# Kernel tuning notes

Hardware: AMD Instinct MI355X
Metric: run time of the kernel (lower is better)

## Reference

```python
import jax, jax.numpy as jnp
import numpy as np

R, C, B, E, H = 128, 256, 1, 768, 12
DK = E // H

def setup_inputs() -> dict:
    key = jax.random.key(0)
    ks = jax.random.split(key, 5)
    s = 1.0 / np.sqrt(E)
    return {
        "x": jax.random.normal(ks[0], (R, C, B, E), jnp.float32),
        "Wq": jax.random.normal(ks[1], (E, E), jnp.float32) * s,
        "bq": jnp.zeros((E,), jnp.float32),
        "Wk": jax.random.normal(ks[2], (E, E), jnp.float32) * s,
        "bk": jnp.zeros((E,), jnp.float32),
        "Wv": jax.random.normal(ks[3], (E, E), jnp.float32) * s,
        "bv": jnp.zeros((E,), jnp.float32),
        "Wo": jax.random.normal(ks[4], (E, E), jnp.float32) * s,
        "bo": jnp.zeros((E,), jnp.float32),
    }

def reference(x, Wq, bq, Wk, bk, Wv, bv, Wo, bo):
    n_rows, n_cols, batch, emb = x.shape
    scaling = (DK ** -0.5) / jnp.sqrt(jnp.float32(n_rows))
    # projections (torch Linear: x @ W.T + b)
    q = (x @ Wq.T + bq).reshape(n_rows, n_cols, batch, H, DK) * scaling
    k = (x @ Wk.T + bk).reshape(n_rows, n_cols, batch, H, DK)
    v = (x @ Wv.T + bv).reshape(n_rows, n_cols, batch, H, DK)
    # pooled attention logits: sum over rows r -> [H, B, C, C]
    attn = jnp.einsum('rinhd,rjnhd->hnij', q, k)
    probs = jax.nn.softmax(attn, axis=-1)  # single softmax shared across rows
    # context: [R, C, B, H, DK]
    c = jnp.einsum('hnij,rjnhd->rinhd', probs, v).reshape(n_rows, n_cols, batch, emb)
    out = c @ Wo.T + bo
    return out, probs
```

## Files before the change

### kernel.cpp

```cpp
#include <hip/hip_runtime.h>
#include <math.h>

#define R_  128
#define C_  256
#define E_  768
#define H_  12
#define DK_ 64
#define T_  (R_*C_)
#define RS_ 8
#define LP  40

typedef __attribute__((ext_vector_type(8))) short          bf16x8;
typedef __attribute__((ext_vector_type(4))) float          f32x4;
typedef __attribute__((ext_vector_type(4))) unsigned short u16x4;
typedef __attribute__((ext_vector_type(8))) unsigned short u16x8;

struct HL { unsigned short h, l; };

__device__ __forceinline__ HL split2(float f) {
    HL o;
    unsigned int u = __float_as_uint(f);
    o.h = (unsigned short)(u >> 16);
    float r = f - __uint_as_float(u & 0xFFFF0000u);
    o.l = (unsigned short)(__float_as_uint(r) >> 16);
    return o;
}

__device__ __forceinline__ void gload16(const void* g, void* l) {
    __builtin_amdgcn_global_load_lds(
        (const __attribute__((address_space(1))) unsigned int*)g,
        (__attribute__((address_space(3))) unsigned int*)l,
        16, 0, 0);
}

__global__ __launch_bounds__(256) void split_kernel(
    const float* __restrict__ src,
    unsigned short* __restrict__ h, unsigned short* __restrict__ l)
{
    const size_t i = ((size_t)blockIdx.x * 256 + threadIdx.x) * 8;
    float4 f0 = *(const float4*)(src + i);
    float4 f1 = *(const float4*)(src + i + 4);
    float v[8] = { f0.x, f0.y, f0.z, f0.w, f1.x, f1.y, f1.z, f1.w };
    u16x8 hh, ll;
    #pragma unroll
    for (int j = 0; j < 8; ++j) { HL e = split2(v[j]); hh[j] = e.h; ll[j] = e.l; }
    *(u16x8*)(h + i) = hh;
    *(u16x8*)(l + i) = ll;
}

template<int OMODE>
__global__ __launch_bounds__(256, 2) void gemm_kernel(
    const unsigned short* __restrict__ Ah, const unsigned short* __restrict__ Al,
    const unsigned short* __restrict__ Bh, const unsigned short* __restrict__ Bl,
    const float* __restrict__ bias, float scale,
    float* __restrict__ Y32, unsigned short* __restrict__ Yh, unsigned short* __restrict__ Yl)
{
    __shared__ __align__(16) unsigned short smem[16384];
    const unsigned short* AsH = smem;
    const unsigned short* AsL = smem + 4096;
    const unsigned short* BsH = smem + 8192;
    const unsigned short* BsL = smem + 12288;

    const int tid  = threadIdx.x;
    const int m0   = blockIdx.x * 128;
    const int n0   = blockIdx.y * 128;
    const int wave = tid >> 6, lane = tid & 63;
    const int wm   = (wave & 1) * 64, wn = (wave >> 1) * 64;
    const int fr   = lane & 15;
    const int kqs  = (((lane >> 4) ^ ((fr >> 1) & 3)) * 8);

    const int lrow = lane >> 2;
    const int gd   = (lane & 3) ^ ((lane >> 3) & 3);
    const unsigned short* gsrc = (wave == 0) ? Ah : (wave == 1) ? Al
                               : (wave == 2) ? Bh : Bl;
    const int rbase = (wave < 2) ? m0 : n0;
    unsigned short* lt = smem + wave * 4096;
    const unsigned short* sp = gsrc + (size_t)(rbase + lrow) * E_ + 8 * gd;

    f32x4 acc[4][4] = {};

    for (int k0 = 0; k0 < E_; k0 += 32) {
        #pragma unroll
        for (int i = 0; i < 8; ++i)
            gload16(sp + k0 + (size_t)i * 16 * E_, lt + i * 512);
        __syncthreads();

        bf16x8 a_h[4], a_l[4], b_h[4], b_l[4];
        #pragma unroll
        for (int t = 0; t < 4; ++t) {
            a_h[t] = *(const bf16x8*)&AsH[(wm + t * 16 + fr) * 32 + kqs];
            a_l[t] = *(const bf16x8*)&AsL[(wm + t * 16 + fr) * 32 + kqs];
            b_h[t] = *(const bf16x8*)&BsH[(wn + t * 16 + fr) * 32 + kqs];
            b_l[t] = *(const bf16x8*)&BsL[(wn + t * 16 + fr) * 32 + kqs];
        }
        #pragma unroll
        for (int i = 0; i < 4; ++i)
            #pragma unroll
            for (int j = 0; j < 4; ++j) {
                acc[i][j] = __builtin_amdgcn_mfma_f32_16x16x32_bf16(a_h[i], b_h[j], acc[i][j], 0, 0, 0);
                acc[i][j] = __builtin_amdgcn_mfma_f32_16x16x32_bf16(a_h[i], b_l[j], acc[i][j], 0, 0, 0);
                acc[i][j] = __builtin_amdgcn_mfma_f32_16x16x32_bf16(a_l[i], b_h[j], acc[i][j], 0, 0, 0);
            }
        __syncthreads();
    }

    float* rep = (float*)smem + wave * 1024;
    const int mr = lane >> 2;
    const int nc = (lane & 3) * 16;
    #pragma unroll
    for (int ti = 0; ti < 4; ++ti) {
        __syncthreads();
        #pragma unroll
        for (int tj = 0; tj < 4; ++tj)
            #pragma unroll
            for (int r = 0; r < 4; ++r)
                rep[((lane >> 4) * 4 + r) * 64 + tj * 16 + fr] = acc[ti][tj][r];
        __syncthreads();
        float v[16];
        #pragma unroll
        for (int c = 0; c < 4; ++c)
            *(float4*)&v[4 * c] = *(const float4*)&rep[mr * 64 + nc + 4 * c];
        const int gm = m0 + wm + ti * 16 + mr;
        const int gn = n0 + wn + nc;
        if constexpr (OMODE == 1) {
            #pragma unroll
            for (int c = 0; c < 4; ++c) {
                float4 bv = *(const float4*)&bias[gn + 4 * c];
                float4 o;
                o.x = (v[4*c+0] + bv.x) * scale; o.y = (v[4*c+1] + bv.y) * scale;
                o.z = (v[4*c+2] + bv.z) * scale; o.w = (v[4*c+3] + bv.w) * scale;
                *(float4*)&Y32[(size_t)gm * E_ + gn + 4 * c] = o;
            }
        } else {
            unsigned short hh[16], ll[16];
            #pragma unroll
            for (int c = 0; c < 4; ++c) {
                float4 bv = *(const float4*)&bias[gn + 4 * c];
                HL e0 = split2((v[4*c+0] + bv.x) * scale);
                HL e1 = split2((v[4*c+1] + bv.y) * scale);
                HL e2 = split2((v[4*c+2] + bv.z) * scale);
                HL e3 = split2((v[4*c+3] + bv.w) * scale);
                hh[4*c+0] = e0.h; ll[4*c+0] = e0.l;
                hh[4*c+1] = e1.h; ll[4*c+1] = e1.l;
                hh[4*c+2] = e2.h; ll[4*c+2] = e2.l;
                hh[4*c+3] = e3.h; ll[4*c+3] = e3.l;
            }
            u16x8 H0, H1, L0, L1;
            #pragma unroll
            for (int j = 0; j < 8; ++j) { H0[j] = hh[j]; H1[j] = hh[8+j]; L0[j] = ll[j]; L1[j] = ll[8+j]; }
            *(u16x8*)&Yh[(size_t)gm * E_ + gn]     = H0;
            *(u16x8*)&Yh[(size_t)gm * E_ + gn + 8] = H1;
            *(u16x8*)&Yl[(size_t)gm * E_ + gn]     = L0;
            *(u16x8*)&Yl[(size_t)gm * E_ + gn + 8] = L1;
        }
    }
}

__global__ __launch_bounds__(256, 2) void attn_mfma(
    const unsigned short* __restrict__ Qh, const unsigned short* __restrict__ Ql,
    const unsigned short* __restrict__ Kh, const unsigned short* __restrict__ Kl,
    float* __restrict__ part)
{
    __shared__ __align__(16) unsigned short smem[16384];
    const unsigned short* AsH = smem;
    const unsigned short* AsL = smem + 4096;
    const unsigned short* BsH = smem + 8192;
    const unsigned short* BsL = smem + 12288;

    const int tid  = threadIdx.x;
    const int i0   = blockIdx.x * 128;
    const int j0   = blockIdx.y * 128;
    const int hz   = blockIdx.z;
    const int h    = hz >> 3;
    const int rc   = hz & 7;
    const int wave = tid >> 6, lane = tid & 63;
    const int wm   = (wave & 1) * 64, wn = (wave >> 1) * 64;
    const int fr   = lane & 15;
    const int kqs  = (((lane >> 4) ^ ((fr >> 1) & 3)) * 8);

    const int lrow = lane >> 2;
    const int gd   = (lane & 3) ^ ((lane >> 3) & 3);
    const unsigned short* gsrc = (wave == 0) ? Qh : (wave == 1) ? Ql
                               : (wave == 2) ? Kh : Kl;
    const int rbase = (wave < 2) ? i0 : j0;
    unsigned short* lt = smem + wave * 4096;

    f32x4 acc[4][4] = {};

    for (int s = 0; s < 32; ++s) {
        const int r  = rc * 16 + (s >> 1);
        const int d0 = (s & 1) * 32;
        const unsigned short* sp =
            gsrc + ((size_t)(r * C_) + rbase + lrow) * E_ + h * DK_ + d0 + 8 * gd;
        #pragma unroll
        for (int i = 0; i < 8; ++i)
            gload16(sp + (size_t)i * 16 * E_, lt + i * 512);
        __syncthreads();

        bf16x8 a_h[4], a_l[4], b_h[4], b_l[4];
        #pragma unroll
        for (int t = 0; t < 4; ++t) {
            a_h[t] = *(const bf16x8*)&AsH[(wm + t * 16 + fr) * 32 + kqs];
            a_l[t] = *(const bf16x8*)&AsL[(wm + t * 16 + fr) * 32 + kqs];
            b_h[t] = *(const bf16x8*)&BsH[(wn + t * 16 + fr) * 32 + kqs];
            b_l[t] = *(const bf16x8*)&BsL[(wn + t * 16 + fr) * 32 + kqs];
        }
        #pragma unroll
        for (int i = 0; i < 4; ++i)
            #pragma unroll
            for (int j = 0; j < 4; ++j) {
                acc[i][j] = __builtin_amdgcn_mfma_f32_16x16x32_bf16(a_h[i], b_h[j], acc[i][j], 0, 0, 0);
                acc[i][j] = __builtin_amdgcn_mfma_f32_16x16x32_bf16(a_h[i], b_l[j], acc[i][j], 0, 0, 0);
                acc[i][j] = __builtin_amdgcn_mfma_f32_16x16x32_bf16(a_l[i], b_h[j], acc[i][j], 0, 0, 0);
            }
        __syncthreads();
    }

    float* rep = (float*)smem + wave * 1024;
    const int mr = lane >> 2;
    const int nc = (lane & 3) * 16;
    #pragma unroll
    for (int ti = 0; ti < 4; ++ti) {
        __syncthreads();
        #pragma unroll
        for (int tj = 0; tj < 4; ++tj)
            #pragma unroll
            for (int r = 0; r < 4; ++r)
                rep[((lane >> 4) * 4 + r) * 64 + tj * 16 + fr] = acc[ti][tj][r];
        __syncthreads();
        const int gi = i0 + wm + ti * 16 + mr;
        const int gj = j0 + wn + nc;
        #pragma unroll
        for (int c = 0; c < 4; ++c) {
            float4 o = *(const float4*)&rep[mr * 64 + nc + 4 * c];
            *(float4*)&part[((size_t)(rc * H_ + h) * C_ + gi) * C_ + gj + 4 * c] = o;
        }
    }
}

__global__ __launch_bounds__(256) void softmax_split(
    const float* __restrict__ part, float* __restrict__ probs,
    unsigned short* __restrict__ ph, unsigned short* __restrict__ pl)
{
    const int row = blockIdx.x;
    const int j = threadIdx.x;
    const int wave = j >> 6, lane = j & 63;

    float s = 0.0f;
    #pragma unroll
    for (int rcn = 0; rcn < RS_; ++rcn)
        s += part[((size_t)rcn * H_ * C_ + row) * C_ + j];

    float m = s;
    #pragma unroll
    for (int off = 32; off > 0; off >>= 1)
        m = fmaxf(m, __shfl_down(m, off, 64));
    __shared__ float redm[4];
    if (lane == 0) redm[wave] = m;
    __syncthreads();
    m = fmaxf(fmaxf(redm[0], redm[1]), fmaxf(redm[2], redm[3]));

    float e = expf(s - m);
    float t = e;
    #pragma unroll
    for (int off = 32; off > 0; off >>= 1)
        t += __shfl_down(t, off, 64);
    __shared__ float reds[4];
    if (lane == 0) reds[wave] = t;
    __syncthreads();
    t = reds[0] + reds[1] + reds[2] + reds[3];

    float p = e / t;
    probs[(size_t)row * C_ + j] = p;
    HL sp = split2(p);
    ph[(size_t)row * C_ + j] = sp.h;
    pl[(size_t)row * C_ + j] = sp.l;
}

__global__ __launch_bounds__(256, 2) void ctx_mfma(
    const unsigned short* __restrict__ Ph, const unsigned short* __restrict__ Pl,
    const unsigned short* __restrict__ Vh, const unsigned short* __restrict__ Vl,
    unsigned short* __restrict__ Ch, unsigned short* __restrict__ Cl)
{
    __shared__ __align__(16) unsigned short smem[15360];
    unsigned short* PsH = smem;
    unsigned short* PsL = smem + 5120;
    unsigned short* VsH = smem + 10240;
    unsigned short* VsL = smem + 12800;

    const int tid  = threadIdx.x;
    const int i0   = blockIdx.x * 128;
    const int r    = blockIdx.y;
    const int h    = blockIdx.z;
    const int wave = tid >> 6, lane = tid & 63;
    const int wm   = (wave & 1) * 64, wn = (wave >> 1) * 32;
    const int fr   = lane & 15;
    const int kq   = (lane >> 4) * 8;
    const int srow = tid >> 1;
    const int sk   = (tid & 1) * 16;
    const int vjj  = tid & 31;
    const int vdg  = tid >> 5;

    f32x4 acc[4][2] = {};

    for (int s = 0; s < 8; ++s) {
        const int jb = s * 32;
        const size_t pb = ((size_t)(h * C_) + i0 + srow) * C_ + jb + sk;
        *(u16x8*)&PsH[srow * LP + sk]     = *(const u16x8*)&Ph[pb];
        *(u16x8*)&PsH[srow * LP + sk + 8] = *(const u16x8*)&Ph[pb + 8];
        *(u16x8*)&PsL[srow * LP + sk]     = *(const u16x8*)&Pl[pb];
        *(u16x8*)&PsL[srow * LP + sk + 8] = *(const u16x8*)&Pl[pb + 8];
        const size_t vb = ((size_t)(r * C_) + jb + vjj) * E_ + h * DK_ + vdg * 8;
        u16x8 v_h = *(const u16x8*)&Vh[vb];
        u16x8 v_l = *(const u16x8*)&Vl[vb];
        #pragma unroll
        for (int u = 0; u < 8; ++u) {
            VsH[(vdg * 8 + u) * LP + vjj] = v_h[u];
            VsL[(vdg * 8 + u) * LP + vjj] = v_l[u];
        }
        __syncthreads();

        bf16x8 p_h[4], p_l[4], w_h[2], w_l[2];
        #pragma unroll
        for (int t = 0; t < 4; ++t) {
            p_h[t] = *(const bf16x8*)&PsH[(wm + t * 16 + fr) * LP + kq];
            p_l[t] = *(const bf16x8*)&PsL[(wm + t * 16 + fr) * LP + kq];
        }
        #pragma unroll
        for (int t = 0; t < 2; ++t) {
            w_h[t] = *(const bf16x8*)&VsH[(wn + t * 16 + fr) * LP + kq];
            w_l[t] = *(const bf16x8*)&VsL[(wn + t * 16 + fr) * LP + kq];
        }
        #pragma unroll
        for (int i = 0; i < 4; ++i)
            #pragma unroll
            for (int j = 0; j < 2; ++j) {
                acc[i][j] = __builtin_amdgcn_mfma_f32_16x16x32_bf16(p_h[i], w_h[j], acc[i][j], 0, 0, 0);
                acc[i][j] = __builtin_amdgcn_mfma_f32_16x16x32_bf16(p_h[i], w_l[j], acc[i][j], 0, 0, 0);
                acc[i][j] = __builtin_amdgcn_mfma_f32_16x16x32_bf16(p_l[i], w_h[j], acc[i][j], 0, 0, 0);
            }
        __syncthreads();
    }

    float* rep = (float*)smem + wave * 512;
    const int mr = lane >> 2;
    const int nc = (lane & 3) * 8;
    #pragma unroll
    for (int ti = 0; ti < 4; ++ti) {
        __syncthreads();
        #pragma unroll
        for (int tj = 0; tj < 2; ++tj)
            #pragma unroll
            for (int rr = 0; rr < 4; ++rr)
                rep[((lane >> 4) * 4 + rr) * 32 + tj * 16 + fr] = acc[ti][tj][rr];
        __syncthreads();
        float v[8];
        *(float4*)&v[0] = *(const float4*)&rep[mr * 32 + nc];
        *(float4*)&v[4] = *(const float4*)&rep[mr * 32 + nc + 4];
        const int gm = r * C_ + i0 + wm + ti * 16 + mr;
        const int gn = h * DK_ + wn + nc;
        u16x8 H8, L8;
        #pragma unroll
        for (int jj = 0; jj < 8; ++jj) { HL e = split2(v[jj]); H8[jj] = e.h; L8[jj] = e.l; }
        *(u16x8*)&Ch[(size_t)gm * E_ + gn] = H8;
        *(u16x8*)&Cl[(size_t)gm * E_ + gn] = L8;
    }
}

extern "C" void kernel_launch(void* const* d_in, const int* in_sizes, int n_in,
                              void* d_out, int out_size, void* d_ws, size_t ws_size,
                              hipStream_t stream)
{
    (void)in_sizes; (void)n_in; (void)out_size; (void)ws_size;

    const float* x  = (const float*)d_in[0];
    const float* Wq = (const float*)d_in[1];
    const float* bq = (const float*)d_in[2];
    const float* Wk = (const float*)d_in[3];
    const float* bk = (const float*)d_in[4];
    const float* Wv = (const float*)d_in[5];
    const float* bv = (const float*)d_in[6];
    const float* Wo = (const float*)d_in[7];
    const float* bo = (const float*)d_in[8];

    float* out   = (float*)d_out;
    float* probs = out + (size_t)T_ * E_;
    float* part  = out;

    const size_t QN = (size_t)T_ * E_;
    const size_t WN = (size_t)E_ * E_;
    unsigned short* qh = (unsigned short*)d_ws;
    unsigned short* ql = qh + QN;
    unsigned short* kh = ql + QN;
    unsigned short* kl = kh + QN;
    unsigned short* vh = kl + QN;
    unsigned short* vl = vh + QN;
    unsigned short* ph = kh;
    unsigned short* pl = kh + (size_t)H_ * C_ * C_;
    unsigned short* ch = qh;
    unsigned short* cl = ql;

    unsigned short* xh   = (unsigned short*)out;
    unsigned short* xl   = xh + QN;
    unsigned short* wsph = (unsigned short*)probs;
    unsigned short* wspl = wsph + WN;
    unsigned short* woh  = kl;
    unsigned short* wol  = kl + WN;

    const float scaling = 0.125f / sqrtf(128.0f);

    dim3 blk(256);
    const int xblocks = (int)(QN / 2048);
    const int wblocks = (int)(WN / 2048);

    split_kernel<<<dim3(xblocks), blk, 0, stream>>>(x, xh, xl);

    split_kernel<<<dim3(wblocks), blk, 0, stream>>>(Wq, wsph, wspl);
    gemm_kernel<0><<<dim3(T_ / 128, E_ / 128), blk, 0, stream>>>(
        xh, xl, wsph, wspl, bq, scaling, nullptr, qh, ql);

    split_kernel<<<dim3(wblocks), blk, 0, stream>>>(Wk, wsph, wspl);
    gemm_kernel<0><<<dim3(T_ / 128, E_ / 128), blk, 0, stream>>>(
        xh, xl, wsph, wspl, bk, 1.0f, nullptr, kh, kl);

    split_kernel<<<dim3(wblocks), blk, 0, stream>>>(Wv, wsph, wspl);
    gemm_kernel<0><<<dim3(T_ / 128, E_ / 128), blk, 0, stream>>>(
        xh, xl, wsph, wspl, bv, 1.0f, nullptr, vh, vl);

    attn_mfma<<<dim3(C_ / 128, C_ / 128, H_ * RS_), blk, 0, stream>>>(qh, ql, kh, kl, part);

    split_kernel<<<dim3(wblocks), blk, 0, stream>>>(Wo, woh, wol);

    softmax_split<<<dim3(H_ * C_), blk, 0, stream>>>(part, probs, ph, pl);
    ctx_mfma<<<dim3(C_ / 128, R_, H_), blk, 0, stream>>>(ph, pl, vh, vl, ch, cl);

    gemm_kernel<1><<<dim3(T_ / 128, E_ / 128), blk, 0, stream>>>(
        ch, cl, woh, wol, bo, 1.0f, out, nullptr, nullptr);
}
```

Before: 915.3 us.

## Double-buffer LDS tiles in GEMM and attention-logit kernels to prefetch next K-slice

Both the projection GEMM and the pooled attention-logit kernel now use two LDS buffers. The global-to-LDS load for the next K step is issued right after the barrier, before the MFMA work on the current buffer runs. This is meant to hide global load latency behind matrix math and removes one barrier per iteration. In exchange, LDS per block doubles to 64 KB, which may limit occupancy or change how many blocks fit per CU.

```diff
diff --git a/kernel.cpp b/kernel.cpp
--- a/kernel.cpp
+++ b/kernel.cpp
@@ -55,11 +55,7 @@
     const float* __restrict__ bias, float scale,
     float* __restrict__ Y32, unsigned short* __restrict__ Yh, unsigned short* __restrict__ Yl)
 {
-    __shared__ __align__(16) unsigned short smem[16384];
-    const unsigned short* AsH = smem;
-    const unsigned short* AsL = smem + 4096;
-    const unsigned short* BsH = smem + 8192;
-    const unsigned short* BsL = smem + 12288;
+    __shared__ __align__(16) unsigned short smem[2][16384];
 
     const int tid  = threadIdx.x;
     const int m0   = blockIdx.x * 128;
@@ -74,16 +70,31 @@
     const unsigned short* gsrc = (wave == 0) ? Ah : (wave == 1) ? Al
                                : (wave == 2) ? Bh : Bl;
     const int rbase = (wave < 2) ? m0 : n0;
-    unsigned short* lt = smem + wave * 4096;
     const unsigned short* sp = gsrc + (size_t)(rbase + lrow) * E_ + 8 * gd;
+    const int ltoff = wave * 4096;
 
     f32x4 acc[4][4] = {};
 
+    {
+        unsigned short* lt = &smem[0][ltoff];
+        #pragma unroll
+        for (int i = 0; i < 8; ++i)
+            gload16(sp + (size_t)i * 16 * E_, lt + i * 512);
+    }
+
+    int cur = 0;
     for (int k0 = 0; k0 < E_; k0 += 32) {
-        #pragma unroll
-        for (int i = 0; i < 8; ++i)
-            gload16(sp + k0 + (size_t)i * 16 * E_, lt + i * 512);
-        __syncthreads();
+        __syncthreads();
+        if (k0 + 32 < E_) {
+            unsigned short* lt = &smem[cur ^ 1][ltoff];
+            #pragma unroll
+            for (int i = 0; i < 8; ++i)
+                gload16(sp + k0 + 32 + (size_t)i * 16 * E_, lt + i * 512);
+        }
+        const unsigned short* AsH = smem[cur];
+        const unsigned short* AsL = smem[cur] + 4096;
+        const unsigned short* BsH = smem[cur] + 8192;
+        const unsigned short* BsL = smem[cur] + 12288;
 
         bf16x8 a_h[4], a_l[4], b_h[4], b_l[4];
         #pragma unroll
@@ -101,10 +112,10 @@
                 acc[i][j] = __builtin_amdgcn_mfma_f32_16x16x32_bf16(a_h[i], b_l[j], acc[i][j], 0, 0, 0);
                 acc[i][j] = __builtin_amdgcn_mfma_f32_16x16x32_bf16(a_l[i], b_h[j], acc[i][j], 0, 0, 0);
             }
-        __syncthreads();
-    }
-
-    float* rep = (float*)smem + wave * 1024;
+        cur ^= 1;
+    }
+
+    float* rep = (float*)&smem[0][0] + wave * 1024;
     const int mr = lane >> 2;
     const int nc = (lane & 3) * 16;
     #pragma unroll
@@ -161,11 +172,7 @@
     const unsigned short* __restrict__ Kh, const unsigned short* __restrict__ Kl,
     float* __restrict__ part)
 {
-    __shared__ __align__(16) unsigned short smem[16384];
-    const unsigned short* AsH = smem;
-    const unsigned short* AsL = smem + 4096;
-    const unsigned short* BsH = smem + 8192;
-    const unsigned short* BsL = smem + 12288;
+    __shared__ __align__(16) unsigned short smem[2][16384];
 
     const int tid  = threadIdx.x;
     const int i0   = blockIdx.x * 128;
@@ -183,19 +190,35 @@
     const unsigned short* gsrc = (wave == 0) ? Qh : (wave == 1) ? Ql
                                : (wave == 2) ? Kh : Kl;
     const int rbase = (wave < 2) ? i0 : j0;
-    unsigned short* lt = smem + wave * 4096;
+    const int ltoff = wave * 4096;
+    const unsigned short* sp0 =
+        gsrc + ((size_t)(rc * 16 * C_) + rbase + lrow) * E_ + h * DK_ + 8 * gd;
 
     f32x4 acc[4][4] = {};
 
+    {
+        unsigned short* lt = &smem[0][ltoff];
+        #pragma unroll
+        for (int i = 0; i < 8; ++i)
+            gload16(sp0 + (size_t)i * 16 * E_, lt + i * 512);
+    }
+
+    int cur = 0;
     for (int s = 0; s < 32; ++s) {
-        const int r  = rc * 16 + (s >> 1);
-        const int d0 = (s & 1) * 32;
-        const unsigned short* sp =
-            gsrc + ((size_t)(r * C_) + rbase + lrow) * E_ + h * DK_ + d0 + 8 * gd;
-        #pragma unroll
-        for (int i = 0; i < 8; ++i)
-            gload16(sp + (size_t)i * 16 * E_, lt + i * 512);
-        __syncthreads();
+        __syncthreads();
+        if (s + 1 < 32) {
+            const int sn = s + 1;
+            const unsigned short* sp =
+                sp0 + (size_t)(sn >> 1) * C_ * E_ + (sn & 1) * 32;
+            unsigned short* lt = &smem[cur ^ 1][ltoff];
+            #pragma unroll
+            for (int i = 0; i < 8; ++i)
+                gload16(sp + (size_t)i * 16 * E_, lt + i * 512);
+        }
+        const unsigned short* AsH = smem[cur];
+        const unsigned short* AsL = smem[cur] + 4096;
+        const unsigned short* BsH = smem[cur] + 8192;
+        const unsigned short* BsL = smem[cur] + 12288;
 
         bf16x8 a_h[4], a_l[4], b_h[4], b_l[4];
         #pragma unroll
@@ -213,10 +236,10 @@
                 acc[i][j] = __builtin_amdgcn_mfma_f32_16x16x32_bf16(a_h[i], b_l[j], acc[i][j], 0, 0, 0);
                 acc[i][j] = __builtin_amdgcn_mfma_f32_16x16x32_bf16(a_l[i], b_h[j], acc[i][j], 0, 0, 0);
             }
-        __syncthreads();
-    }
-
-    float* rep = (float*)smem + wave * 1024;
+        cur ^= 1;
+    }
+
+    float* rep = (float*)&smem[0][0] + wave * 1024;
     const int mr = lane >> 2;
     const int nc = (lane & 3) * 16;
     #pragma unroll
```

Measured after the change: 873.6 us. 4.6% less time.
